# Performance work log

Hardware: AMD Instinct MI355X
Metric: run time of the kernel (lower is better)

Reference implementation:

```python
import jax, jax.numpy as jnp
import numpy as np

N = 100000      # nodes
E = 1600000     # edges (no self-loops by construction)
DIN, DH, DOUT = 128, 128, 64
EPS = 1e-8      # torch cosine_similarity eps
LN_EPS = 1e-5


def _segsum(v, idx, n=N):
    return jax.ops.segment_sum(v, idx, num_segments=n)


def att_coef(feats, row, col):
    """Edge-wise cosine-sim attention + degree norm + self-loop append (torch no_grad block).
    Returns fixed-shape (row2, col2, vals2) of length E+N; filtered edges get weight 0
    (equivalent to removal for all scatter_add / message-passing math)."""
    dot = jnp.einsum('ed,ed->e', feats[row], feats[col])            # [E]
    nrm = jnp.maximum(jnp.linalg.norm(feats, axis=1), EPS)          # [N]
    sims = dot / (nrm[row] * nrm[col])
    keep = sims >= 0.1                                              # row!=col guaranteed
    sims = jnp.where(keep, sims, 0.0)
    deg = _segsum(sims, row)
    dinv = jnp.where(deg > 0, deg ** -0.5, 0.0)                     # inf -> 0
    sims = dinv[row] * sims * dinv[col]
    deg_new = _segsum(keep.astype(feats.dtype), col) + 1.0          # [N], >= 1
    self_val = 1.0 / deg_new
    vals = jnp.where(keep, jnp.exp(sims), 0.0)                      # removed edges -> 0
    sl = jnp.arange(N)
    row2 = jnp.concatenate([row, sl])
    col2 = jnp.concatenate([col, sl])
    vals2 = jnp.concatenate([vals, jnp.exp(self_val)])
    return row2, col2, vals2


def gcn_conv(x, row, col, w, W, b):
    """PyG GCNConv (normalize=True, add_self_loops=False) with given edge_weight."""
    h = x @ W                                                        # [N, out]
    deg = _segsum(w, col)
    dinv = jnp.where(deg > 0, deg ** -0.5, 0.0)
    norm = dinv[row] * w * dinv[col]                                 # [E+N]
    out = _segsum(norm[:, None] * h[row], col)                       # scatter to targets
    return out + b


def layer_norm(x, g, b):
    mu = jnp.mean(x, axis=-1, keepdims=True)
    var = jnp.mean((x - mu) ** 2, axis=-1, keepdims=True)
    return (x - mu) * jax.lax.rsqrt(var + LN_EPS) * g + b


def setup_inputs() -> dict:
    key = jax.random.key(0)
    ks = jax.random.split(key, 6)
    x = jax.random.normal(ks[0], (N, DIN), jnp.float32)
    row = jax.random.randint(ks[1], (E,), 0, N)
    col = jax.random.randint(ks[2], (E,), 0, N)
    col = jnp.where(col == row, (col + 1) % N, col)                  # no self-loops
    s1 = float(np.sqrt(6.0 / (DIN + DH)))                            # glorot
    s2 = float(np.sqrt(6.0 / (DH + DOUT)))
    W1 = jax.random.uniform(ks[3], (DIN, DH), jnp.float32, -s1, s1)
    W2 = jax.random.uniform(ks[4], (DH, DOUT), jnp.float32, -s2, s2)
    return dict(x=x, row=row, col=col,
                W1=W1, b1=jnp.zeros((DH,), jnp.float32),
                ln_g=jnp.ones((DH,), jnp.float32), ln_b=jnp.zeros((DH,), jnp.float32),
                W2=W2, b2=jnp.zeros((DOUT,), jnp.float32))


def reference(x, row, col, W1, b1, ln_g, ln_b, W2, b2):
    # layer 1: att_coef (no_grad) -> GCNConv -> LayerNorm -> ReLU (dropout is eval no-op)
    r2, c2, v2 = att_coef(jax.lax.stop_gradient(x), row, col)
    h = gcn_conv(x, r2, c2, v2, W1, b1)
    h = jax.nn.relu(layer_norm(h, ln_g, ln_b))
    # layer 2: att_coef on updated features (original edge list), final conv + log_softmax
    r2, c2, v2 = att_coef(jax.lax.stop_gradient(h), row, col)
    out = gcn_conv(h, r2, c2, v2, W2, b2)
    return jax.nn.log_softmax(out, axis=-1)
```

## Files before the change

kernel.cpp:

```cpp
#include <hip/hip_runtime.h>
#include <math.h>

#define EPSF 1e-8f
#define LN_EPS 1e-5f
#define BL_MARGIN 0.002f

typedef unsigned int  u32;
typedef unsigned short u16;
typedef _Float16 h2_t __attribute__((ext_vector_type(2)));

static __device__ inline u32 pack_h2(float a, float b) {
    h2_t h; h.x = (_Float16)a; h.y = (_Float16)b;
    return __builtin_bit_cast(u32, h);
}
static __device__ inline float h2lo(u32 u) {
    return (float)__builtin_bit_cast(h2_t, u).x;
}
static __device__ inline float h2hi(u32 u) {
    return (float)__builtin_bit_cast(h2_t, u).y;
}
static __device__ inline float fdot2_u32(u32 a, u32 b, float c) {
    return __builtin_amdgcn_fdot2(__builtin_bit_cast(h2_t, a),
                                  __builtin_bit_cast(h2_t, b), c, false);
}

__global__ __launch_bounds__(256) void cast_norm_k(const float* __restrict__ feat,
    u32* __restrict__ fhf, float* __restrict__ nrm, int n) {
    int wid  = (blockIdx.x * 256 + threadIdx.x) >> 6;
    int lane = threadIdx.x & 63;
    if (wid >= n) return;
    float2 v = *(const float2*)(feat + (size_t)wid * 128 + lane * 2);
    float s = v.x * v.x + v.y * v.y;
    #pragma unroll
    for (int off = 32; off; off >>= 1) s += __shfl_xor(s, off, 64);
    float nv = fmaxf(sqrtf(s), EPSF);
    float inv = 1.0f / nv;
    fhf[(size_t)wid * 64 + lane] = pack_h2(v.x * inv, v.y * inv);
    if (lane == 0) nrm[wid] = nv;
}


__global__ __launch_bounds__(256) void count_k(const int* __restrict__ col,
                                               int* __restrict__ cntAll, int ecnt) {
    int e = blockIdx.x * 256 + threadIdx.x;
    if (e < ecnt) atomicAdd(&cntAll[col[e]], 1);
}

__global__ __launch_bounds__(256) void scan1_k(const int* __restrict__ cnt,
    int* __restrict__ colStart, int* __restrict__ bsum, int n) {
    __shared__ int tmp[256];
    int i = blockIdx.x * 256 + threadIdx.x;
    int v = (i < n) ? cnt[i] : 0;
    tmp[threadIdx.x] = v; __syncthreads();
    for (int off = 1; off < 256; off <<= 1) {
        int t = (threadIdx.x >= off) ? tmp[threadIdx.x - off] : 0;
        __syncthreads();
        tmp[threadIdx.x] += t;
        __syncthreads();
    }
    if (i < n) colStart[i] = tmp[threadIdx.x] - v;
    if (threadIdx.x == 255) bsum[blockIdx.x] = tmp[255];
}

__global__ __launch_bounds__(512) void scan2_k(int* __restrict__ bsum, int nb) {
    __shared__ int tmp[512];
    int v = (threadIdx.x < nb) ? bsum[threadIdx.x] : 0;
    tmp[threadIdx.x] = v; __syncthreads();
    for (int off = 1; off < 512; off <<= 1) {
        int t = (threadIdx.x >= off) ? tmp[threadIdx.x - off] : 0;
        __syncthreads();
        tmp[threadIdx.x] += t;
        __syncthreads();
    }
    if (threadIdx.x < nb) bsum[threadIdx.x] = tmp[threadIdx.x] - v;
}

__global__ __launch_bounds__(256) void scan3_k(int* __restrict__ colStart,
    const int* __restrict__ bsum, int n) {
    int i = blockIdx.x * 256 + threadIdx.x;
    if (i < n) colStart[i] += bsum[blockIdx.x];
}

__global__ __launch_bounds__(256) void fill_k(const int* __restrict__ row,
    const int* __restrict__ col, const int* __restrict__ startAll,
    int* __restrict__ cur, int* __restrict__ rowAll, int ecnt) {
    int e = blockIdx.x * 256 + threadIdx.x;
    if (e >= ecnt) return;
    int c = col[e];
    int p = startAll[c] + atomicAdd(&cur[c], 1);
    rowAll[p] = row[e];
}

__global__ __launch_bounds__(256) void edge_dot_hf_k(const u32* __restrict__ fhf,
    const float* __restrict__ feat32,
    const int* __restrict__ rowAll, const int* __restrict__ startAll,
    const int* __restrict__ cntAll, const float* __restrict__ nrm,
    float* __restrict__ sims, float* __restrict__ deg1, int n) {
    int wid  = (blockIdx.x * 256 + threadIdx.x) >> 6;
    int lane = threadIdx.x & 63;
    if (wid >= n) return;
    int s0 = startAll[wid], cnt = cntAll[wid];
    if (cnt == 0) return;
    int q = lane >> 4, l = lane & 15;
    uint4 fc = *(const uint4*)(fhf + (size_t)wid * 64 + l * 4);
    float nc = nrm[wid];
    int cm1 = cnt - 1;
    for (int jj = 0; jj < cnt; jj += 16) {
        int j0 = jj + q, j1 = j0 + 4, j2 = j0 + 8, j3 = j0 + 12;
        bool a0 = j0 < cnt, a1 = j1 < cnt, a2 = j2 < cnt, a3 = j3 < cnt;
        int r0 = rowAll[s0 + min(j0, cm1)];
        int r1 = rowAll[s0 + min(j1, cm1)];
        int r2 = rowAll[s0 + min(j2, cm1)];
        int r3 = rowAll[s0 + min(j3, cm1)];
        uint4 f0 = *(const uint4*)(fhf + (size_t)r0 * 64 + l * 4);
        uint4 f1 = *(const uint4*)(fhf + (size_t)r1 * 64 + l * 4);
        uint4 f2 = *(const uint4*)(fhf + (size_t)r2 * 64 + l * 4);
        uint4 f3 = *(const uint4*)(fhf + (size_t)r3 * 64 + l * 4);
        float p0 = fdot2_u32(f0.x, fc.x, 0.0f);
        float p1 = fdot2_u32(f1.x, fc.x, 0.0f);
        float p2 = fdot2_u32(f2.x, fc.x, 0.0f);
        float p3 = fdot2_u32(f3.x, fc.x, 0.0f);
        p0 = fdot2_u32(f0.y, fc.y, p0); p1 = fdot2_u32(f1.y, fc.y, p1);
        p2 = fdot2_u32(f2.y, fc.y, p2); p3 = fdot2_u32(f3.y, fc.y, p3);
        p0 = fdot2_u32(f0.z, fc.z, p0); p1 = fdot2_u32(f1.z, fc.z, p1);
        p2 = fdot2_u32(f2.z, fc.z, p2); p3 = fdot2_u32(f3.z, fc.z, p3);
        p0 = fdot2_u32(f0.w, fc.w, p0); p1 = fdot2_u32(f1.w, fc.w, p1);
        p2 = fdot2_u32(f2.w, fc.w, p2); p3 = fdot2_u32(f3.w, fc.w, p3);
        #pragma unroll
        for (int off = 8; off; off >>= 1) {
            p0 += __shfl_xor(p0, off, 64);
            p1 += __shfl_xor(p1, off, 64);
            p2 += __shfl_xor(p2, off, 64);
            p3 += __shfl_xor(p3, off, 64);
        }
        if (a0 && fabsf(p0 - 0.1f) < BL_MARGIN) {
            const float4* fr = (const float4*)(feat32 + (size_t)r0 * 128);
            const float4* fq = (const float4*)(feat32 + (size_t)wid * 128);
            float4 x0 = fr[l*2], x1 = fr[l*2+1], y0 = fq[l*2], y1 = fq[l*2+1];
            float s2 = x0.x*y0.x + x0.y*y0.y + x0.z*y0.z + x0.w*y0.w
                     + x1.x*y1.x + x1.y*y1.y + x1.z*y1.z + x1.w*y1.w;
            #pragma unroll
            for (int off = 8; off; off >>= 1) s2 += __shfl_xor(s2, off, 64);
            p0 = s2 / (nrm[r0] * nc);
        }
        if (a1 && fabsf(p1 - 0.1f) < BL_MARGIN) {
            const float4* fr = (const float4*)(feat32 + (size_t)r1 * 128);
            const float4* fq = (const float4*)(feat32 + (size_t)wid * 128);
            float4 x0 = fr[l*2], x1 = fr[l*2+1], y0 = fq[l*2], y1 = fq[l*2+1];
            float s2 = x0.x*y0.x + x0.y*y0.y + x0.z*y0.z + x0.w*y0.w
                     + x1.x*y1.x + x1.y*y1.y + x1.z*y1.z + x1.w*y1.w;
            #pragma unroll
            for (int off = 8; off; off >>= 1) s2 += __shfl_xor(s2, off, 64);
            p1 = s2 / (nrm[r1] * nc);
        }
        if (a2 && fabsf(p2 - 0.1f) < BL_MARGIN) {
            const float4* fr = (const float4*)(feat32 + (size_t)r2 * 128);
            const float4* fq = (const float4*)(feat32 + (size_t)wid * 128);
            float4 x0 = fr[l*2], x1 = fr[l*2+1], y0 = fq[l*2], y1 = fq[l*2+1];
            float s2 = x0.x*y0.x + x0.y*y0.y + x0.z*y0.z + x0.w*y0.w
                     + x1.x*y1.x + x1.y*y1.y + x1.z*y1.z + x1.w*y1.w;
            #pragma unroll
            for (int off = 8; off; off >>= 1) s2 += __shfl_xor(s2, off, 64);
            p2 = s2 / (nrm[r2] * nc);
        }
        if (a3 && fabsf(p3 - 0.1f) < BL_MARGIN) {
            const float4* fr = (const float4*)(feat32 + (size_t)r3 * 128);
            const float4* fq = (const float4*)(feat32 + (size_t)wid * 128);
            float4 x0 = fr[l*2], x1 = fr[l*2+1], y0 = fq[l*2], y1 = fq[l*2+1];
            float s2 = x0.x*y0.x + x0.y*y0.y + x0.z*y0.z + x0.w*y0.w
                     + x1.x*y1.x + x1.y*y1.y + x1.z*y1.z + x1.w*y1.w;
            #pragma unroll
            for (int off = 8; off; off >>= 1) s2 += __shfl_xor(s2, off, 64);
            p3 = s2 / (nrm[r3] * nc);
        }
        if (l == 0) {
            if (a0) {
                float kv = (p0 >= 0.1f) ? p0 : 0.0f;
                sims[s0 + j0] = kv;
                if (kv > 0.0f) atomicAdd(&deg1[r0], kv);
            }
            if (a1) {
                float kv = (p1 >= 0.1f) ? p1 : 0.0f;
                sims[s0 + j1] = kv;
                if (kv > 0.0f) atomicAdd(&deg1[r1], kv);
            }
            if (a2) {
                float kv = (p2 >= 0.1f) ? p2 : 0.0f;
                sims[s0 + j2] = kv;
                if (kv > 0.0f) atomicAdd(&deg1[r2], kv);
            }
            if (a3) {
                float kv = (p3 >= 0.1f) ? p3 : 0.0f;
                sims[s0 + j3] = kv;
                if (kv > 0.0f) atomicAdd(&deg1[r3], kv);
            }
        }
    }
}

__global__ __launch_bounds__(256) void edge_c_csr_k(const float* __restrict__ sims,
    const int* __restrict__ rowAll, const int* __restrict__ startAll,
    const int* __restrict__ cntAll, const float* __restrict__ deg1,
    int2* __restrict__ kv, int* __restrict__ cntK, float* __restrict__ dinv2,
    float* __restrict__ cself, int n) {
    int wid  = (blockIdx.x * 256 + threadIdx.x) >> 6;
    int lane = threadIdx.x & 63;
    if (wid >= n) return;
    int s0 = startAll[wid], cnt = cntAll[wid];
    float degc = deg1[wid];
    float d1c = (degc > 0.0f) ? 1.0f / sqrtf(degc) : 0.0f;
    float vsum = 0.0f; int kc = 0;
    for (int jj = 0; jj < cnt; jj += 64) {
        int j = jj + lane;
        bool keep = false; int r = 0; float v = 0.0f;
        if (j < cnt) {
            float s = sims[s0 + j];
            if (s > 0.0f) {
                r = rowAll[s0 + j];
                float dr = 1.0f / sqrtf(deg1[r]);
                v = expf(dr * s * d1c);
                keep = true;
            }
        }
        unsigned long long m = __ballot(keep ? 1 : 0);
        if (keep) {
            int pre = __popcll(m & ((1ull << lane) - 1ull));
            int2 pk; pk.x = r; pk.y = __float_as_int(v);
            kv[s0 + kc + pre] = pk;
            vsum += v;
        }
        kc += __popcll(m);
    }
    #pragma unroll
    for (int off = 32; off; off >>= 1) vsum += __shfl_xor(vsum, off, 64);
    if (lane == 0) {
        float ws_ = expf(1.0f / ((float)kc + 1.0f));
        float dg = ws_ + vsum;
        float di = 1.0f / sqrtf(dg);
        dinv2[wid] = di;
        cself[wid] = di * ws_;
        cntK[wid]  = kc;
    }
}


__global__ __launch_bounds__(256) void gemm128_k(const float* __restrict__ A,
    const float* __restrict__ W, const float* __restrict__ scale,
    float* __restrict__ out, int n) {
    __shared__ float Ws[128 * 64];
    int colBase = blockIdx.y * 64;
    for (int i = threadIdx.x; i < 128 * 64 / 4; i += 256) {
        int k = i >> 4, c4 = i & 15;
        ((float4*)Ws)[i] = *(const float4*)(W + k * 128 + colBase + c4 * 4);
    }
    __syncthreads();
    const int TPN = 16;
    int group = threadIdx.x / TPN;
    int tin   = threadIdx.x % TPN;
    int nid   = (blockIdx.x * 16 + group) * 4;
    if (nid >= n) return;
    int dbase = tin * 4;
    int nm1 = n - 1;
    const float4* a0 = (const float4*)(A + (size_t)min(nid,     nm1) * 128);
    const float4* a1 = (const float4*)(A + (size_t)min(nid + 1, nm1) * 128);
    const float4* a2 = (const float4*)(A + (size_t)min(nid + 2, nm1) * 128);
    const float4* a3 = (const float4*)(A + (size_t)min(nid + 3, nm1) * 128);
    float4 acc0 = {0,0,0,0}, acc1 = {0,0,0,0}, acc2 = {0,0,0,0}, acc3 = {0,0,0,0};
    #pragma unroll 2
    for (int k4 = 0; k4 < 32; ++k4) {
        const float* wr = Ws + (k4 * 4) * 64 + dbase;
        float4 w0 = *(const float4*)(wr);
        float4 w1 = *(const float4*)(wr + 64);
        float4 w2 = *(const float4*)(wr + 128);
        float4 w3 = *(const float4*)(wr + 192);
        float4 v0 = a0[k4], v1 = a1[k4], v2 = a2[k4], v3 = a3[k4];
        acc0.x += v0.x*w0.x + v0.y*w1.x + v0.z*w2.x + v0.w*w3.x;
        acc0.y += v0.x*w0.y + v0.y*w1.y + v0.z*w2.y + v0.w*w3.y;
        acc0.z += v0.x*w0.z + v0.y*w1.z + v0.z*w2.z + v0.w*w3.z;
        acc0.w += v0.x*w0.w + v0.y*w1.w + v0.z*w2.w + v0.w*w3.w;
        acc1.x += v1.x*w0.x + v1.y*w1.x + v1.z*w2.x + v1.w*w3.x;
        acc1.y += v1.x*w0.y + v1.y*w1.y + v1.z*w2.y + v1.w*w3.y;
        acc1.z += v1.x*w0.z + v1.y*w1.z + v1.z*w2.z + v1.w*w3.z;
        acc1.w += v1.x*w0.w + v1.y*w1.w + v1.z*w2.w + v1.w*w3.w;
        acc2.x += v2.x*w0.x + v2.y*w1.x + v2.z*w2.x + v2.w*w3.x;
        acc2.y += v2.x*w0.y + v2.y*w1.y + v2.z*w2.y + v2.w*w3.y;
        acc2.z += v2.x*w0.z + v2.y*w1.z + v2.z*w2.z + v2.w*w3.z;
        acc2.w += v2.x*w0.w + v2.y*w1.w + v2.z*w2.w + v2.w*w3.w;
        acc3.x += v3.x*w0.x + v3.y*w1.x + v3.z*w2.x + v3.w*w3.x;
        acc3.y += v3.x*w0.y + v3.y*w1.y + v3.z*w2.y + v3.w*w3.y;
        acc3.z += v3.x*w0.z + v3.y*w1.z + v3.z*w2.z + v3.w*w3.z;
        acc3.w += v3.x*w0.w + v3.y*w1.w + v3.z*w2.w + v3.w*w3.w;
    }
    float4 accs[4] = {acc0, acc1, acc2, acc3};
    #pragma unroll
    for (int i = 0; i < 4; ++i) {
        if (nid + i < n) {
            float sc = scale[nid + i];
            float4 r; r.x = accs[i].x * sc; r.y = accs[i].y * sc;
            r.z = accs[i].z * sc; r.w = accs[i].w * sc;
            *(float4*)(out + (size_t)(nid + i) * 128 + colBase + dbase) = r;
        }
    }
}

__global__ __launch_bounds__(256) void gemm64_hf_k(const float* __restrict__ A,
    const float* __restrict__ W, const float* __restrict__ scale,
    u32* __restrict__ outhf, int n) {
    __shared__ float Ws[128 * 32];
    int colBase = blockIdx.y * 32;
    for (int i = threadIdx.x; i < 128 * 32 / 4; i += 256) {
        int k = i >> 3, c4 = i & 7;
        ((float4*)Ws)[i] = *(const float4*)(W + k * 64 + colBase + c4 * 4);
    }
    __syncthreads();
    const int TPN = 8;
    int group = threadIdx.x / TPN;
    int tin   = threadIdx.x % TPN;
    int nid   = (blockIdx.x * 32 + group) * 4;
    if (nid >= n) return;
    int dbase = tin * 4;
    int nm1 = n - 1;
    const float4* a0 = (const float4*)(A + (size_t)min(nid,     nm1) * 128);
    const float4* a1 = (const float4*)(A + (size_t)min(nid + 1, nm1) * 128);
    const float4* a2 = (const float4*)(A + (size_t)min(nid + 2, nm1) * 128);
    const float4* a3 = (const float4*)(A + (size_t)min(nid + 3, nm1) * 128);
    float4 acc0 = {0,0,0,0}, acc1 = {0,0,0,0}, acc2 = {0,0,0,0}, acc3 = {0,0,0,0};
    #pragma unroll 2
    for (int k4 = 0; k4 < 32; ++k4) {
        const float* wr = Ws + (k4 * 4) * 32 + dbase;
        float4 w0 = *(const float4*)(wr);
        float4 w1 = *(const float4*)(wr + 32);
        float4 w2 = *(const float4*)(wr + 64);
        float4 w3 = *(const float4*)(wr + 96);
        float4 v0 = a0[k4], v1 = a1[k4], v2 = a2[k4], v3 = a3[k4];
        acc0.x += v0.x*w0.x + v0.y*w1.x + v0.z*w2.x + v0.w*w3.x;
        acc0.y += v0.x*w0.y + v0.y*w1.y + v0.z*w2.y + v0.w*w3.y;
        acc0.z += v0.x*w0.z + v0.y*w1.z + v0.z*w2.z + v0.w*w3.z;
        acc0.w += v0.x*w0.w + v0.y*w1.w + v0.z*w2.w + v0.w*w3.w;
        acc1.x += v1.x*w0.x + v1.y*w1.x + v1.z*w2.x + v1.w*w3.x;
        acc1.y += v1.x*w0.y + v1.y*w1.y + v1.z*w2.y + v1.w*w3.y;
        acc1.z += v1.x*w0.z + v1.y*w1.z + v1.z*w2.z + v1.w*w3.z;
        acc1.w += v1.x*w0.w + v1.y*w1.w + v1.z*w2.w + v1.w*w3.w;
        acc2.x += v2.x*w0.x + v2.y*w1.x + v2.z*w2.x + v2.w*w3.x;
        acc2.y += v2.x*w0.y + v2.y*w1.y + v2.z*w2.y + v2.w*w3.y;
        acc2.z += v2.x*w0.z + v2.y*w1.z + v2.z*w2.z + v2.w*w3.z;
        acc2.w += v2.x*w0.w + v2.y*w1.w + v2.z*w2.w + v2.w*w3.w;
        acc3.x += v3.x*w0.x + v3.y*w1.x + v3.z*w2.x + v3.w*w3.x;
        acc3.y += v3.x*w0.y + v3.y*w1.y + v3.z*w2.y + v3.w*w3.y;
        acc3.z += v3.x*w0.z + v3.y*w1.z + v3.z*w2.z + v3.w*w3.z;
        acc3.w += v3.x*w0.w + v3.y*w1.w + v3.z*w2.w + v3.w*w3.w;
    }
    float4 accs[4] = {acc0, acc1, acc2, acc3};
    #pragma unroll
    for (int i = 0; i < 4; ++i) {
        if (nid + i < n) {
            float sc = scale[nid + i];
            u32 o0 = pack_h2(accs[i].x * sc, accs[i].y * sc);
            u32 o1 = pack_h2(accs[i].z * sc, accs[i].w * sc);
            *(uint2*)(outhf + (size_t)(nid + i) * 32 + (colBase >> 1) + tin * 2)
                = make_uint2(o0, o1);
        }
    }
}


__global__ __launch_bounds__(256) void gather_ln_k(const float* __restrict__ hs,
    const int2* __restrict__ kv, const int* __restrict__ startAll,
    const int* __restrict__ cntK, const float* __restrict__ dinv2,
    const float* __restrict__ cself, const float* __restrict__ bias,
    const float* __restrict__ g, const float* __restrict__ bln,
    float* __restrict__ outbuf, u32* __restrict__ outhf,
    float* __restrict__ nrm, int n) {
    int wid = (blockIdx.x * 256 + threadIdx.x) >> 5;
    int l   = threadIdx.x & 31;
    if (wid >= n) return;
    int s0 = startAll[wid], k = cntK[wid];
    float4 acc = {0,0,0,0};
    int j = 0;
    for (; j + 7 < k; j += 8) {
        int2 p0 = kv[s0+j],   p1 = kv[s0+j+1], p2 = kv[s0+j+2], p3 = kv[s0+j+3];
        int2 p4 = kv[s0+j+4], p5 = kv[s0+j+5], p6 = kv[s0+j+6], p7 = kv[s0+j+7];
        float4 h0 = *(const float4*)(hs + (size_t)p0.x * 128 + l * 4);
        float4 h1 = *(const float4*)(hs + (size_t)p1.x * 128 + l * 4);
        float4 h2v = *(const float4*)(hs + (size_t)p2.x * 128 + l * 4);
        float4 h3 = *(const float4*)(hs + (size_t)p3.x * 128 + l * 4);
        float4 h4 = *(const float4*)(hs + (size_t)p4.x * 128 + l * 4);
        float4 h5 = *(const float4*)(hs + (size_t)p5.x * 128 + l * 4);
        float4 h6 = *(const float4*)(hs + (size_t)p6.x * 128 + l * 4);
        float4 h7 = *(const float4*)(hs + (size_t)p7.x * 128 + l * 4);
        float v0 = __int_as_float(p0.y), v1 = __int_as_float(p1.y);
        float v2 = __int_as_float(p2.y), v3 = __int_as_float(p3.y);
        float v4 = __int_as_float(p4.y), v5 = __int_as_float(p5.y);
        float v6 = __int_as_float(p6.y), v7 = __int_as_float(p7.y);
        acc.x += v0*h0.x + v1*h1.x + v2*h2v.x + v3*h3.x
               + v4*h4.x + v5*h5.x + v6*h6.x + v7*h7.x;
        acc.y += v0*h0.y + v1*h1.y + v2*h2v.y + v3*h3.y
               + v4*h4.y + v5*h5.y + v6*h6.y + v7*h7.y;
        acc.z += v0*h0.z + v1*h1.z + v2*h2v.z + v3*h3.z
               + v4*h4.z + v5*h5.z + v6*h6.z + v7*h7.z;
        acc.w += v0*h0.w + v1*h1.w + v2*h2v.w + v3*h3.w
               + v4*h4.w + v5*h5.w + v6*h6.w + v7*h7.w;
    }
    for (; j < k; ++j) {
        int2 p0 = kv[s0 + j];
        float4 h0 = *(const float4*)(hs + (size_t)p0.x * 128 + l * 4);
        float v0 = __int_as_float(p0.y);
        acc.x += v0*h0.x; acc.y += v0*h0.y; acc.z += v0*h0.z; acc.w += v0*h0.w;
    }
    float di = dinv2[wid], cs = cself[wid];
    float4 hsv = *(const float4*)(hs + (size_t)wid * 128 + l * 4);
    float4 vb  = *(const float4*)(bias + l * 4);
    float x0 = di*acc.x + cs*hsv.x + vb.x;
    float x1 = di*acc.y + cs*hsv.y + vb.y;
    float x2 = di*acc.z + cs*hsv.z + vb.z;
    float x3 = di*acc.w + cs*hsv.w + vb.w;
    float s = x0 + x1 + x2 + x3;
    #pragma unroll
    for (int off = 16; off; off >>= 1) s += __shfl_xor(s, off, 64);
    float mu = s * (1.0f / 128.0f);
    float d0 = x0 - mu, d1 = x1 - mu, d2 = x2 - mu, d3 = x3 - mu;
    float vv = d0*d0 + d1*d1 + d2*d2 + d3*d3;
    #pragma unroll
    for (int off = 16; off; off >>= 1) vv += __shfl_xor(vv, off, 64);
    float rstd = 1.0f / sqrtf(vv * (1.0f / 128.0f) + LN_EPS);
    float4 vg  = *(const float4*)(g + l * 4);
    float4 vbl = *(const float4*)(bln + l * 4);
    float y0 = fmaxf(d0 * rstd * vg.x + vbl.x, 0.0f);
    float y1 = fmaxf(d1 * rstd * vg.y + vbl.y, 0.0f);
    float y2 = fmaxf(d2 * rstd * vg.z + vbl.z, 0.0f);
    float y3 = fmaxf(d3 * rstd * vg.w + vbl.w, 0.0f);
    float4 yo; yo.x = y0; yo.y = y1; yo.z = y2; yo.w = y3;
    *(float4*)(outbuf + (size_t)wid * 128 + l * 4) = yo;
    float ns = y0*y0 + y1*y1 + y2*y2 + y3*y3;
    #pragma unroll
    for (int off = 16; off; off >>= 1) ns += __shfl_xor(ns, off, 64);
    float nv = fmaxf(sqrtf(ns), EPSF);
    float inv = 1.0f / nv;
    uint2 oh; oh.x = pack_h2(y0 * inv, y1 * inv); oh.y = pack_h2(y2 * inv, y3 * inv);
    *(uint2*)(outhf + (size_t)wid * 64 + l * 2) = oh;
    if (l == 0) nrm[wid] = nv;
}

__global__ __launch_bounds__(256) void gather_lsm_hf_k(const u32* __restrict__ g2s,
    const int2* __restrict__ kv, const int* __restrict__ startAll,
    const int* __restrict__ cntK, const float* __restrict__ dinv2,
    const float* __restrict__ cself, const float* __restrict__ b2,
    float* __restrict__ out, int n) {
    int wid = (blockIdx.x * 256 + threadIdx.x) >> 5;
    int l   = threadIdx.x & 31;
    if (wid >= n) return;
    int s0 = startAll[wid], k = cntK[wid];
    float acc0 = 0.f, acc1 = 0.f;
    int j = 0;
    for (; j + 7 < k; j += 8) {
        int2 p0 = kv[s0+j],   p1 = kv[s0+j+1], p2 = kv[s0+j+2], p3 = kv[s0+j+3];
        int2 p4 = kv[s0+j+4], p5 = kv[s0+j+5], p6 = kv[s0+j+6], p7 = kv[s0+j+7];
        u32 g0 = g2s[(size_t)p0.x * 32 + l];
        u32 g1 = g2s[(size_t)p1.x * 32 + l];
        u32 g2 = g2s[(size_t)p2.x * 32 + l];
        u32 g3 = g2s[(size_t)p3.x * 32 + l];
        u32 g4 = g2s[(size_t)p4.x * 32 + l];
        u32 g5 = g2s[(size_t)p5.x * 32 + l];
        u32 g6 = g2s[(size_t)p6.x * 32 + l];
        u32 g7 = g2s[(size_t)p7.x * 32 + l];
        float v0 = __int_as_float(p0.y), v1 = __int_as_float(p1.y);
        float v2 = __int_as_float(p2.y), v3 = __int_as_float(p3.y);
        float v4 = __int_as_float(p4.y), v5 = __int_as_float(p5.y);
        float v6 = __int_as_float(p6.y), v7 = __int_as_float(p7.y);
        acc0 += v0*h2lo(g0) + v1*h2lo(g1) + v2*h2lo(g2) + v3*h2lo(g3)
              + v4*h2lo(g4) + v5*h2lo(g5) + v6*h2lo(g6) + v7*h2lo(g7);
        acc1 += v0*h2hi(g0) + v1*h2hi(g1) + v2*h2hi(g2) + v3*h2hi(g3)
              + v4*h2hi(g4) + v5*h2hi(g5) + v6*h2hi(g6) + v7*h2hi(g7);
    }
    for (; j < k; ++j) {
        int2 p0 = kv[s0 + j];
        u32 g0 = g2s[(size_t)p0.x * 32 + l];
        float v0 = __int_as_float(p0.y);
        acc0 += v0 * h2lo(g0); acc1 += v0 * h2hi(g0);
    }
    float di = dinv2[wid], cs = cself[wid];
    u32 gsu = g2s[(size_t)wid * 32 + l];
    float2 vb = *(const float2*)(b2 + l * 2);
    float v0 = di * acc0 + cs * h2lo(gsu) + vb.x;
    float v1 = di * acc1 + cs * h2hi(gsu) + vb.y;
    float m = fmaxf(v0, v1);
    #pragma unroll
    for (int off = 16; off; off >>= 1) m = fmaxf(m, __shfl_xor(m, off, 64));
    float e = expf(v0 - m) + expf(v1 - m);
    #pragma unroll
    for (int off = 16; off; off >>= 1) e += __shfl_xor(e, off, 64);
    float lse = m + logf(e);
    *(float2*)(out + (size_t)wid * 64 + l * 2) = make_float2(v0 - lse, v1 - lse);
}


extern "C" void kernel_launch(void* const* d_in, const int* in_sizes, int n_in,
                              void* d_out, int out_size, void* d_ws, size_t ws_size,
                              hipStream_t stream) {
    (void)n_in; (void)out_size; (void)ws_size;
    const float* x   = (const float*)d_in[0];
    const int*   row = (const int*)d_in[1];
    const int*   col = (const int*)d_in[2];
    const float* W1  = (const float*)d_in[3];
    const float* b1  = (const float*)d_in[4];
    const float* lng = (const float*)d_in[5];
    const float* lnb = (const float*)d_in[6];
    const float* W2  = (const float*)d_in[7];
    const float* b2  = (const float*)d_in[8];
    float* out = (float*)d_out;

    const int N = in_sizes[0] / 128;
    const int E = in_sizes[1];

    int*   cntAll   = (int*)d_ws;
    int*   startAll = cntAll + N;
    int*   bsum     = startAll + N;
    float* nrm      = (float*)(bsum + 512);
    float* deg1     = nrm + N;
    float* dinv2    = deg1 + N;
    float* cself    = dinv2 + N;
    int*   cntK     = (int*)(cself + N);
    int*   rowAll   = cntK + N;
    int2*  kvp      = (int2*)(rowAll + E);
    u32*   fhf      = (u32*)(kvp + E);
    u32*   g2shf    = fhf + (size_t)64 * N;
    float* big      = (float*)(g2shf + (size_t)32 * N);
    float* sims     = big;
    float* hs       = big;
    float* h2       = big + (size_t)128 * N;

    const int nodeBlocks  = (N + 255) / 256;
    const int waveBlocks  = (N + 3) / 4;
    const int halfBlocks  = (N + 7) / 8;
    const int edgeBlocks  = (E + 255) / 256;
    const int scanBlocks  = nodeBlocks;

    hipMemsetAsync(cntAll, 0, (size_t)N * sizeof(int), stream);
    count_k<<<edgeBlocks, 256, 0, stream>>>(col, cntAll, E);
    scan1_k<<<scanBlocks, 256, 0, stream>>>(cntAll, startAll, bsum, N);
    scan2_k<<<1, 512, 0, stream>>>(bsum, scanBlocks);
    scan3_k<<<scanBlocks, 256, 0, stream>>>(startAll, bsum, N);
    hipMemsetAsync(cntK, 0, (size_t)N * sizeof(int), stream);
    fill_k<<<edgeBlocks, 256, 0, stream>>>(row, col, startAll, cntK, rowAll, E);

    hipMemsetAsync(deg1, 0, (size_t)N * sizeof(float), stream);
    cast_norm_k<<<waveBlocks, 256, 0, stream>>>(x, fhf, nrm, N);
    edge_dot_hf_k<<<waveBlocks, 256, 0, stream>>>(fhf, x, rowAll, startAll, cntAll, nrm,
                                                  sims, deg1, N);
    edge_c_csr_k<<<waveBlocks, 256, 0, stream>>>(sims, rowAll, startAll, cntAll, deg1,
                                                 kvp, cntK, dinv2, cself, N);
    gemm128_k<<<dim3((N + 63) / 64, 2), 256, 0, stream>>>(x, W1, dinv2, hs, N);
    gather_ln_k<<<halfBlocks, 256, 0, stream>>>(hs, kvp, startAll, cntK, dinv2, cself,
                                                b1, lng, lnb, h2, fhf, nrm, N);

    hipMemsetAsync(deg1, 0, (size_t)N * sizeof(float), stream);
    edge_dot_hf_k<<<waveBlocks, 256, 0, stream>>>(fhf, h2, rowAll, startAll, cntAll, nrm,
                                                  sims, deg1, N);
    edge_c_csr_k<<<waveBlocks, 256, 0, stream>>>(sims, rowAll, startAll, cntAll, deg1,
                                                 kvp, cntK, dinv2, cself, N);
    gemm64_hf_k<<<dim3((N + 127) / 128, 2), 256, 0, stream>>>(h2, W2, dinv2, g2shf, N);
    gather_lsm_hf_k<<<halfBlocks, 256, 0, stream>>>(g2shf, kvp, startAll, cntK, dinv2,
                                                    cself, b2, out, N);
}
```

Measured before the change: 708.0 us.

## Compute edge cosine dots with MFMA and ballot-driven borderline refinement

Replaces the per-edge fdot2 dot products and shuffle reductions in the edge similarity kernel with 16x16x32 f16 MFMA instructions. The target node's feature vector is broadcast as the A operand and 16 neighbour rows per MFMA form the B operand, processing 32 edges per iteration. The fp32 recomputation for edges near the 0.1 threshold now uses a wave-wide ballot loop across all 64 lanes instead of per-slot branches. This cuts reduction shuffles and ALU work, but computes a full 16x16 tile of which only one column is used.

```diff
diff --git a/kernel.cpp b/kernel.cpp
--- a/kernel.cpp
+++ b/kernel.cpp
@@ -8,6 +8,8 @@
 typedef unsigned int  u32;
 typedef unsigned short u16;
 typedef _Float16 h2_t __attribute__((ext_vector_type(2)));
+typedef _Float16 half8_t __attribute__((ext_vector_type(8)));
+typedef float f32x4_t __attribute__((ext_vector_type(4)));
 
 static __device__ inline u32 pack_h2(float a, float b) {
     h2_t h; h.x = (_Float16)a; h.y = (_Float16)b;
@@ -19,9 +21,10 @@
 static __device__ inline float h2hi(u32 u) {
     return (float)__builtin_bit_cast(h2_t, u).y;
 }
-static __device__ inline float fdot2_u32(u32 a, u32 b, float c) {
-    return __builtin_amdgcn_fdot2(__builtin_bit_cast(h2_t, a),
-                                  __builtin_bit_cast(h2_t, b), c, false);
+
+static __device__ inline f32x4_t mfma16(uint4 a, uint4 b, f32x4_t c) {
+    return __builtin_amdgcn_mfma_f32_16x16x32_f16(
+        __builtin_bit_cast(half8_t, a), __builtin_bit_cast(half8_t, b), c, 0, 0, 0);
 }
 
 __global__ __launch_bounds__(256) void cast_norm_k(const float* __restrict__ feat,
@@ -91,7 +94,7 @@
     rowAll[p] = row[e];
 }
 
-__global__ __launch_bounds__(256) void edge_dot_hf_k(const u32* __restrict__ fhf,
+__global__ __launch_bounds__(256) void edge_dot_mf_k(const u32* __restrict__ fhf,
     const float* __restrict__ feat32,
     const int* __restrict__ rowAll, const int* __restrict__ startAll,
     const int* __restrict__ cntAll, const float* __restrict__ nrm,
@@ -101,99 +104,86 @@
     if (wid >= n) return;
     int s0 = startAll[wid], cnt = cntAll[wid];
     if (cnt == 0) return;
-    int q = lane >> 4, l = lane & 15;
-    uint4 fc = *(const uint4*)(fhf + (size_t)wid * 64 + l * 4);
+    int lr = lane & 15;
+    int kq = lane >> 4;
+    const u32* fcp = fhf + (size_t)wid * 64 + kq * 4;
+    uint4 a0 = *(const uint4*)(fcp);
+    uint4 a1 = *(const uint4*)(fcp + 16);
+    uint4 a2 = *(const uint4*)(fcp + 32);
+    uint4 a3 = *(const uint4*)(fcp + 48);
     float nc = nrm[wid];
     int cm1 = cnt - 1;
-    for (int jj = 0; jj < cnt; jj += 16) {
-        int j0 = jj + q, j1 = j0 + 4, j2 = j0 + 8, j3 = j0 + 12;
-        bool a0 = j0 < cnt, a1 = j1 < cnt, a2 = j2 < cnt, a3 = j3 < cnt;
-        int r0 = rowAll[s0 + min(j0, cm1)];
-        int r1 = rowAll[s0 + min(j1, cm1)];
-        int r2 = rowAll[s0 + min(j2, cm1)];
-        int r3 = rowAll[s0 + min(j3, cm1)];
-        uint4 f0 = *(const uint4*)(fhf + (size_t)r0 * 64 + l * 4);
-        uint4 f1 = *(const uint4*)(fhf + (size_t)r1 * 64 + l * 4);
-        uint4 f2 = *(const uint4*)(fhf + (size_t)r2 * 64 + l * 4);
-        uint4 f3 = *(const uint4*)(fhf + (size_t)r3 * 64 + l * 4);
-        float p0 = fdot2_u32(f0.x, fc.x, 0.0f);
-        float p1 = fdot2_u32(f1.x, fc.x, 0.0f);
-        float p2 = fdot2_u32(f2.x, fc.x, 0.0f);
-        float p3 = fdot2_u32(f3.x, fc.x, 0.0f);
-        p0 = fdot2_u32(f0.y, fc.y, p0); p1 = fdot2_u32(f1.y, fc.y, p1);
-        p2 = fdot2_u32(f2.y, fc.y, p2); p3 = fdot2_u32(f3.y, fc.y, p3);
-        p0 = fdot2_u32(f0.z, fc.z, p0); p1 = fdot2_u32(f1.z, fc.z, p1);
-        p2 = fdot2_u32(f2.z, fc.z, p2); p3 = fdot2_u32(f3.z, fc.z, p3);
-        p0 = fdot2_u32(f0.w, fc.w, p0); p1 = fdot2_u32(f1.w, fc.w, p1);
-        p2 = fdot2_u32(f2.w, fc.w, p2); p3 = fdot2_u32(f3.w, fc.w, p3);
-        #pragma unroll
-        for (int off = 8; off; off >>= 1) {
-            p0 += __shfl_xor(p0, off, 64);
-            p1 += __shfl_xor(p1, off, 64);
-            p2 += __shfl_xor(p2, off, 64);
-            p3 += __shfl_xor(p3, off, 64);
-        }
-        if (a0 && fabsf(p0 - 0.1f) < BL_MARGIN) {
-            const float4* fr = (const float4*)(feat32 + (size_t)r0 * 128);
-            const float4* fq = (const float4*)(feat32 + (size_t)wid * 128);
-            float4 x0 = fr[l*2], x1 = fr[l*2+1], y0 = fq[l*2], y1 = fq[l*2+1];
-            float s2 = x0.x*y0.x + x0.y*y0.y + x0.z*y0.z + x0.w*y0.w
-                     + x1.x*y1.x + x1.y*y1.y + x1.z*y1.z + x1.w*y1.w;
+    for (int jj = 0; jj < cnt; jj += 32) {
+        int e1 = jj + lr;
+        int r1 = rowAll[s0 + min(e1, cm1)];
+        const u32* fr1 = fhf + (size_t)r1 * 64 + kq * 4;
+        uint4 b0 = *(const uint4*)(fr1);
+        uint4 b1 = *(const uint4*)(fr1 + 16);
+        uint4 b2 = *(const uint4*)(fr1 + 32);
+        uint4 b3 = *(const uint4*)(fr1 + 48);
+        bool g2 = (jj + 16) < cnt;
+        int e2 = jj + 16 + lr;
+        int r2 = 0;
+        uint4 c0, c1, c2, c3;
+        if (g2) {
+            r2 = rowAll[s0 + min(e2, cm1)];
+            const u32* fr2 = fhf + (size_t)r2 * 64 + kq * 4;
+            c0 = *(const uint4*)(fr2);
+            c1 = *(const uint4*)(fr2 + 16);
+            c2 = *(const uint4*)(fr2 + 32);
+            c3 = *(const uint4*)(fr2 + 48);
+        }
+        f32x4_t acc = {0.f, 0.f, 0.f, 0.f};
+        acc = mfma16(a0, b0, acc);
+        acc = mfma16(a1, b1, acc);
+        acc = mfma16(a2, b2, acc);
+        acc = mfma16(a3, b3, acc);
+        float p1 = acc[0];
+        bool act1 = (kq == 0) && (e1 < cnt);
+        float p2 = 0.0f;
+        bool act2 = false;
+        if (g2) {
+            f32x4_t acc2 = {0.f, 0.f, 0.f, 0.f};
+            acc2 = mfma16(a0, c0, acc2);
+            acc2 = mfma16(a1, c1, acc2);
+            acc2 = mfma16(a2, c2, acc2);
+            acc2 = mfma16(a3, c3, acc2);
+            p2 = acc2[0];
+            act2 = (kq == 0) && (e2 < cnt);
+        }
+        unsigned long long bl = __ballot(act1 && fabsf(p1 - 0.1f) < BL_MARGIN);
+        while (bl) {
+            int src = __ffsll((unsigned long long)bl) - 1; bl &= bl - 1ull;
+            int rt = __shfl(r1, src, 64);
+            float2 xa = *(const float2*)(feat32 + (size_t)rt * 128 + lane * 2);
+            float2 xb = *(const float2*)(feat32 + (size_t)wid * 128 + lane * 2);
+            float s2 = xa.x * xb.x + xa.y * xb.y;
             #pragma unroll
-            for (int off = 8; off; off >>= 1) s2 += __shfl_xor(s2, off, 64);
-            p0 = s2 / (nrm[r0] * nc);
-        }
-        if (a1 && fabsf(p1 - 0.1f) < BL_MARGIN) {
-            const float4* fr = (const float4*)(feat32 + (size_t)r1 * 128);
-            const float4* fq = (const float4*)(feat32 + (size_t)wid * 128);
-            float4 x0 = fr[l*2], x1 = fr[l*2+1], y0 = fq[l*2], y1 = fq[l*2+1];
-            float s2 = x0.x*y0.x + x0.y*y0.y + x0.z*y0.z + x0.w*y0.w
-                     + x1.x*y1.x + x1.y*y1.y + x1.z*y1.z + x1.w*y1.w;
+            for (int off = 32; off; off >>= 1) s2 += __shfl_xor(s2, off, 64);
+            float pf = s2 / (nrm[rt] * nc);
+            if (lane == src) p1 = pf;
+        }
+        unsigned long long bl2 = __ballot(act2 && fabsf(p2 - 0.1f) < BL_MARGIN);
+        while (bl2) {
+            int src = __ffsll((unsigned long long)bl2) - 1; bl2 &= bl2 - 1ull;
+            int rt = __shfl(r2, src, 64);
+            float2 xa = *(const float2*)(feat32 + (size_t)rt * 128 + lane * 2);
+            float2 xb = *(const float2*)(feat32 + (size_t)wid * 128 + lane * 2);
+            float s2 = xa.x * xb.x + xa.y * xb.y;
             #pragma unroll
-            for (int off = 8; off; off >>= 1) s2 += __shfl_xor(s2, off, 64);
-            p1 = s2 / (nrm[r1] * nc);
-        }
-        if (a2 && fabsf(p2 - 0.1f) < BL_MARGIN) {
-            const float4* fr = (const float4*)(feat32 + (size_t)r2 * 128);
-            const float4* fq = (const float4*)(feat32 + (size_t)wid * 128);
-            float4 x0 = fr[l*2], x1 = fr[l*2+1], y0 = fq[l*2], y1 = fq[l*2+1];
-            float s2 = x0.x*y0.x + x0.y*y0.y + x0.z*y0.z + x0.w*y0.w
-                     + x1.x*y1.x + x1.y*y1.y + x1.z*y1.z + x1.w*y1.w;
-            #pragma unroll
-            for (int off = 8; off; off >>= 1) s2 += __shfl_xor(s2, off, 64);
-            p2 = s2 / (nrm[r2] * nc);
-        }
-        if (a3 && fabsf(p3 - 0.1f) < BL_MARGIN) {
-            const float4* fr = (const float4*)(feat32 + (size_t)r3 * 128);
-            const float4* fq = (const float4*)(feat32 + (size_t)wid * 128);
-            float4 x0 = fr[l*2], x1 = fr[l*2+1], y0 = fq[l*2], y1 = fq[l*2+1];
-            float s2 = x0.x*y0.x + x0.y*y0.y + x0.z*y0.z + x0.w*y0.w
-                     + x1.x*y1.x + x1.y*y1.y + x1.z*y1.z + x1.w*y1.w;
-            #pragma unroll
-            for (int off = 8; off; off >>= 1) s2 += __shfl_xor(s2, off, 64);
-            p3 = s2 / (nrm[r3] * nc);
-        }
-        if (l == 0) {
-            if (a0) {
-                float kv = (p0 >= 0.1f) ? p0 : 0.0f;
-                sims[s0 + j0] = kv;
-                if (kv > 0.0f) atomicAdd(&deg1[r0], kv);
-            }
-            if (a1) {
-                float kv = (p1 >= 0.1f) ? p1 : 0.0f;
-                sims[s0 + j1] = kv;
-                if (kv > 0.0f) atomicAdd(&deg1[r1], kv);
-            }
-            if (a2) {
-                float kv = (p2 >= 0.1f) ? p2 : 0.0f;
-                sims[s0 + j2] = kv;
-                if (kv > 0.0f) atomicAdd(&deg1[r2], kv);
-            }
-            if (a3) {
-                float kv = (p3 >= 0.1f) ? p3 : 0.0f;
-                sims[s0 + j3] = kv;
-                if (kv > 0.0f) atomicAdd(&deg1[r3], kv);
-            }
+            for (int off = 32; off; off >>= 1) s2 += __shfl_xor(s2, off, 64);
+            float pf = s2 / (nrm[rt] * nc);
+            if (lane == src) p2 = pf;
+        }
+        if (act1) {
+            float kv = (p1 >= 0.1f) ? p1 : 0.0f;
+            sims[s0 + e1] = kv;
+            if (kv > 0.0f) atomicAdd(&deg1[r1], kv);
+        }
+        if (act2) {
+            float kv = (p2 >= 0.1f) ? p2 : 0.0f;
+            sims[s0 + e2] = kv;
+            if (kv > 0.0f) atomicAdd(&deg1[r2], kv);
         }
     }
 }
@@ -545,7 +535,7 @@
 
     hipMemsetAsync(deg1, 0, (size_t)N * sizeof(float), stream);
     cast_norm_k<<<waveBlocks, 256, 0, stream>>>(x, fhf, nrm, N);
-    edge_dot_hf_k<<<waveBlocks, 256, 0, stream>>>(fhf, x, rowAll, startAll, cntAll, nrm,
+    edge_dot_mf_k<<<waveBlocks, 256, 0, stream>>>(fhf, x, rowAll, startAll, cntAll, nrm,
                                                   sims, deg1, N);
     edge_c_csr_k<<<waveBlocks, 256, 0, stream>>>(sims, rowAll, startAll, cntAll, deg1,
                                                  kvp, cntK, dinv2, cself, N);
@@ -554,7 +544,7 @@
                                                 b1, lng, lnb, h2, fhf, nrm, N);
 
     hipMemsetAsync(deg1, 0, (size_t)N * sizeof(float), stream);
-    edge_dot_hf_k<<<waveBlocks, 256, 0, stream>>>(fhf, h2, rowAll, startAll, cntAll, nrm,
+    edge_dot_mf_k<<<waveBlocks, 256, 0, stream>>>(fhf, h2, rowAll, startAll, cntAll, nrm,
                                                   sims, deg1, N);
     edge_c_csr_k<<<waveBlocks, 256, 0, stream>>>(sims, rowAll, startAll, cntAll, deg1,
                                                  kvp, cntK, dinv2, cself, N);
```

After: 720.0 us. About the same (+1.7%).
